# Optimization experiments

Measured on AMD Instinct MI355X. Metric: run time of the kernel, lower is better.

## Reference

```python
import jax, jax.numpy as jnp
import numpy as np
import math

B, L, D = 2, 2048, 2048
H = 16
HD = D // H  # 128
EPS = 1e-8
ROPE_BASE = 10000.0


def _rms(x, g):
    return x * jax.lax.rsqrt(jnp.mean(x * x, axis=-1, keepdims=True) + EPS) * g


def _rope_tables(seq_len, head_dim, dtype):
    inv_freq = 1.0 / (ROPE_BASE ** (jnp.arange(0, head_dim, 2, dtype=jnp.float32) / head_dim))
    t = jnp.arange(seq_len, dtype=jnp.float32)
    freqs = jnp.outer(t, inv_freq)                 # [L, HD/2]
    emb = jnp.concatenate([freqs, freqs], axis=-1)  # [L, HD]
    return jnp.cos(emb).astype(dtype), jnp.sin(emb).astype(dtype)


def _rotate_half(x):
    x1, x2 = jnp.split(x, 2, axis=-1)
    return jnp.concatenate([-x2, x1], axis=-1)


def setup_inputs() -> dict:
    key = jax.random.key(0)
    ks = jax.random.split(key, 4)
    s = 0.02
    return {
        'x': jax.random.normal(ks[0], (B, L, D), jnp.float32),
        'Wqkv': jax.random.normal(ks[1], (D, 3 * D), jnp.float32) * s,
        'bqkv': jnp.zeros((3 * D,), jnp.float32),
        'Wo': jax.random.normal(ks[2], (D, D), jnp.float32) * s,
        'bo': jnp.zeros((D,), jnp.float32),
        'g1': jnp.ones((D,), jnp.float32),
        'g2': jnp.ones((D,), jnp.float32),
        'Wp': jax.random.normal(ks[3], (D, 8 * D), jnp.float32) * s,
        'bp': jnp.zeros((8 * D,), jnp.float32),
        'Wff_out': jax.random.normal(jax.random.fold_in(key, 7), (4 * D, D), jnp.float32) * s,
        'bff_out': jnp.zeros((D,), jnp.float32),
    }


def reference(x, Wqkv, bqkv, Wo, bo, g1, g2, Wp, bp, Wff_out, bff_out):
    b, l, d = x.shape
    # pre-norm + fused QKV projection
    h = _rms(x, g1)
    qkv = h @ Wqkv + bqkv                                  # [B, L, 3D]
    q, k, v = jnp.split(qkv, 3, axis=-1)
    def heads(t):
        return t.reshape(b, l, H, HD).transpose(0, 2, 1, 3)  # [B, H, L, HD]
    q, k, v = heads(q), heads(k), heads(v)
    # RoPE
    cos, sin = _rope_tables(l, HD, x.dtype)                 # [L, HD]
    cos = cos[None, None]
    sin = sin[None, None]
    q = q * cos + _rotate_half(q) * sin
    k = k * cos + _rotate_half(k) * sin
    # causal SDPA
    scale = 1.0 / math.sqrt(HD)
    scores = jnp.einsum('bhqd,bhkd->bhqk', q, k) * scale
    causal = jnp.tril(jnp.ones((l, l), dtype=bool))
    scores = jnp.where(causal[None, None], scores, jnp.finfo(scores.dtype).min)
    attn = jax.nn.softmax(scores, axis=-1)
    o = jnp.einsum('bhqk,bhkd->bhqd', attn, v)              # [B, H, L, HD]
    o = o.transpose(0, 2, 1, 3).reshape(b, l, d)
    attn_out = o @ Wo + bo
    x = x + attn_out                                        # residual (dropout=0, eval)
    # SwiGLU FFN, pre-norm
    h2 = _rms(x, g2)
    p = h2 @ Wp + bp                                        # [B, L, 8D]
    gate, value = jnp.split(p, 2, axis=-1)
    ff = (jax.nn.silu(gate) * value) @ Wff_out + bff_out
    return x + ff
```

## Files before the change

### kernel.cpp

```cpp
#include <hip/hip_runtime.h>
#include <stdint.h>

typedef unsigned short u16;
typedef float floatx4 __attribute__((ext_vector_type(4)));
typedef short bf16x8 __attribute__((ext_vector_type(8)));

#define DEVI __device__ __forceinline__

#define B_ 2
#define L_ 2048
#define D_ 2048
#define H_ 16
#define HD_ 128
#define M_ 4096

DEVI u16 f2bf(float f) {
  union { float f; uint32_t u; } v; v.f = f;
  uint32_t r = v.u + 0x7fffu + ((v.u >> 16) & 1u);
  return (u16)(r >> 16);
}
DEVI float bf2f(u16 h) {
  union { uint32_t u; float f; } v; v.u = ((uint32_t)h) << 16;
  return v.f;
}

DEVI floatx4 mfma16(bf16x8 a, bf16x8 b, floatx4 c) {
  return __builtin_amdgcn_mfma_f32_16x16x32_bf16(a, b, c, 0, 0, 0);
}

DEVI void gl2lds16(const u16* g, u16* l) {
  __builtin_amdgcn_global_load_lds((const __attribute__((address_space(1))) void*)g,
                                   (__attribute__((address_space(3))) void*)l, 16, 0, 0);
}

__global__ void rmsnorm_kernel(const float* __restrict__ x, const float* __restrict__ g,
                               u16* __restrict__ out) {
  int row = blockIdx.x;
  int tid = threadIdx.x;
  const float* xr = x + (size_t)row * D_;
  float4 v0 = ((const float4*)xr)[tid];
  float4 v1 = ((const float4*)xr)[256 + tid];
  float ss = v0.x*v0.x + v0.y*v0.y + v0.z*v0.z + v0.w*v0.w
           + v1.x*v1.x + v1.y*v1.y + v1.z*v1.z + v1.w*v1.w;
  #pragma unroll
  for (int off = 32; off > 0; off >>= 1) ss += __shfl_xor(ss, off, 64);
  __shared__ float red[4];
  int wv = tid >> 6, ln = tid & 63;
  if (ln == 0) red[wv] = ss;
  __syncthreads();
  float tot = red[0] + red[1] + red[2] + red[3];
  float scale = rsqrtf(tot * (1.0f / (float)D_) + 1e-8f);
  float4 g0 = ((const float4*)g)[tid];
  float4 g1v = ((const float4*)g)[256 + tid];
  u16* orow = out + (size_t)row * D_;
  ushort4 o0, o1;
  o0.x = f2bf(v0.x * scale * g0.x);  o0.y = f2bf(v0.y * scale * g0.y);
  o0.z = f2bf(v0.z * scale * g0.z);  o0.w = f2bf(v0.w * scale * g0.w);
  o1.x = f2bf(v1.x * scale * g1v.x); o1.y = f2bf(v1.y * scale * g1v.y);
  o1.z = f2bf(v1.z * scale * g1v.z); o1.w = f2bf(v1.w * scale * g1v.w);
  ((ushort4*)orow)[tid] = o0;
  ((ushort4*)orow)[256 + tid] = o1;
}

__global__ void transpose_w_kernel(const float* __restrict__ W, u16* __restrict__ Wt,
                                   int Kd, int Nd) {
  __shared__ float tile[32][33];
  int n0 = blockIdx.x * 32, k0 = blockIdx.y * 32;
  int tid = threadIdx.x;
  int r = tid >> 3, c4 = (tid & 7) * 4;
  float4 v = *(const float4*)(W + (size_t)(k0 + r) * Nd + n0 + c4);
  tile[r][c4 + 0] = v.x; tile[r][c4 + 1] = v.y; tile[r][c4 + 2] = v.z; tile[r][c4 + 3] = v.w;
  __syncthreads();
  ushort4 o;
  o.x = f2bf(tile[c4 + 0][r]); o.y = f2bf(tile[c4 + 1][r]);
  o.z = f2bf(tile[c4 + 2][r]); o.w = f2bf(tile[c4 + 3][r]);
  *(ushort4*)(Wt + (size_t)(n0 + r) * Kd + k0 + c4) = o;
}

__global__ void rope_qk_kernel(const u16* __restrict__ qkv, u16* __restrict__ q_r,
                               u16* __restrict__ k_r) {
  int idx = blockIdx.x * 256 + threadIdx.x;
  int i = idx & 63;
  int h = (idx >> 6) & (H_ - 1);
  int l = (idx >> 10) & (L_ - 1);
  int b = idx >> 21;
  float freq = expf(-(float)i * 0.14391156831212787f);
  float ang = (float)l * freq;
  float s, c;
  sincosf(ang, &s, &c);
  size_t base_in = (size_t)(b * L_ + l) * (3 * D_);
  size_t qi = base_in + h * HD_ + i;
  size_t ki = base_in + D_ + h * HD_ + i;
  float q1 = bf2f(qkv[qi]), q2 = bf2f(qkv[qi + 64]);
  float k1 = bf2f(qkv[ki]), k2 = bf2f(qkv[ki + 64]);
  size_t base_out = ((size_t)(b * H_ + h) * L_ + l) * HD_ + i;
  q_r[base_out]      = f2bf(q1 * c - q2 * s);
  q_r[base_out + 64] = f2bf(q2 * c + q1 * s);
  k_r[base_out]      = f2bf(k1 * c - k2 * s);
  k_r[base_out + 64] = f2bf(k2 * c + k1 * s);
}

__global__ void v_transpose_kernel(const u16* __restrict__ qkv, u16* __restrict__ vt) {
  __shared__ u16 tile[32][36];
  int bh = blockIdx.z;
  int d0 = blockIdx.y * 32;
  int l0 = blockIdx.x * 32;
  int b = bh >> 4, h = bh & 15;
  int tid = threadIdx.x;
  int r = tid >> 3, c4 = (tid & 7) * 4;
  const u16* src = qkv + (size_t)(b * L_ + l0 + r) * (3 * D_) + 2 * D_ + h * HD_ + d0 + c4;
  ushort4 v = *(const ushort4*)src;
  tile[r][c4 + 0] = v.x; tile[r][c4 + 1] = v.y; tile[r][c4 + 2] = v.z; tile[r][c4 + 3] = v.w;
  __syncthreads();
  ushort4 o;
  o.x = tile[c4 + 0][r]; o.y = tile[c4 + 1][r]; o.z = tile[c4 + 2][r]; o.w = tile[c4 + 3][r];
  *(ushort4*)(vt + ((size_t)bh * HD_ + d0 + r) * L_ + l0 + c4) = o;
}


template <int MODE>
__launch_bounds__(256, 3)
__global__ void gemm_bt_kernel(const u16* __restrict__ A, const u16* __restrict__ Bt,
                               const float* __restrict__ bias,
                               const float* __restrict__ resid,
                               void* __restrict__ out, int Nn, int Kk) {
  __shared__ __attribute__((aligned(16))) u16 As[128 * 64];
  __shared__ __attribute__((aligned(16))) u16 Bs[128 * 64];
  int tid = threadIdx.x;
  int wave = tid >> 6, lane = tid & 63, quad = lane >> 4, lr = lane & 15;
  int m0 = blockIdx.y * 128, n0 = blockIdx.x * 128;
  int wm = (wave >> 1) * 64, wn = (wave & 1) * 64;
  floatx4 acc[4][4];
  floatx4 z4 = {0.f, 0.f, 0.f, 0.f};
  #pragma unroll
  for (int i = 0; i < 4; i++)
    #pragma unroll
    for (int j = 0; j < 4; j++) acc[i][j] = z4;
  int dr8 = tid >> 3;
  int dg = ((tid & 7) ^ (dr8 & 7)) * 8;
  const u16* Ap = A + (size_t)m0 * Kk;
  const u16* Bp = Bt + (size_t)n0 * Kk;
  for (int kt = 0; kt < Kk; kt += 64) {
    __syncthreads();
    #pragma unroll
    for (int p = 0; p < 4; p++)
      gl2lds16(Ap + (size_t)(p * 32 + dr8) * Kk + kt + dg, As + p * 2048 + tid * 8);
    #pragma unroll
    for (int p = 0; p < 4; p++)
      gl2lds16(Bp + (size_t)(p * 32 + dr8) * Kk + kt + dg, Bs + p * 2048 + tid * 8);
    __syncthreads();
    #pragma unroll
    for (int kk = 0; kk < 2; ++kk) {
      int swz = ((kk * 4 + quad) ^ (lr & 7)) * 8;
      bf16x8 af[4], bfr[4];
      #pragma unroll
      for (int i = 0; i < 4; i++)
        af[i] = *(const bf16x8*)&As[(wm + i * 16 + lr) * 64 + swz];
      #pragma unroll
      for (int i = 0; i < 4; i++)
        bfr[i] = *(const bf16x8*)&Bs[(wn + i * 16 + lr) * 64 + swz];
      #pragma unroll
      for (int mi = 0; mi < 4; mi++)
        #pragma unroll
        for (int ni = 0; ni < 4; ni++)
          acc[mi][ni] = mfma16(af[mi], bfr[ni], acc[mi][ni]);
    }
  }
  #pragma unroll
  for (int mi = 0; mi < 4; mi++) {
    #pragma unroll
    for (int ni = 0; ni < 4; ni++) {
      int col = n0 + wn + ni * 16 + lr;
      float bcol = bias[col];
      #pragma unroll
      for (int r2 = 0; r2 < 4; r2++) {
        int row = m0 + wm + mi * 16 + quad * 4 + r2;
        float v = acc[mi][ni][r2] + bcol;
        size_t off = (size_t)row * Nn + col;
        if (MODE == 0) {
          ((u16*)out)[off] = f2bf(v);
        } else {
          ((float*)out)[off] = v + resid[off];
        }
      }
    }
  }
}

__launch_bounds__(256, 2)
__global__ void ffn_gemm_kernel(const u16* __restrict__ A, const u16* __restrict__ Wt,
                                const float* __restrict__ bp,
                                u16* __restrict__ out, int Kk) {
  __shared__ __attribute__((aligned(16))) u16 As[128 * 64];
  __shared__ __attribute__((aligned(16))) u16 Bg[128 * 64];
  __shared__ __attribute__((aligned(16))) u16 Bv[128 * 64];
  int tid = threadIdx.x;
  int wave = tid >> 6, lane = tid & 63, quad = lane >> 4, lr = lane & 15;
  int m0 = blockIdx.y * 128, n0 = blockIdx.x * 128;
  int wm = (wave >> 1) * 64, wn = (wave & 1) * 64;
  floatx4 accg[4][4], accv[4][4];
  floatx4 z4 = {0.f, 0.f, 0.f, 0.f};
  #pragma unroll
  for (int i = 0; i < 4; i++)
    #pragma unroll
    for (int j = 0; j < 4; j++) { accg[i][j] = z4; accv[i][j] = z4; }
  int dr8 = tid >> 3;
  int dg = ((tid & 7) ^ (dr8 & 7)) * 8;
  const u16* Ap = A + (size_t)m0 * Kk;
  const u16* Bgp = Wt + (size_t)n0 * Kk;
  const u16* Bvp = Wt + (size_t)(8192 + n0) * Kk;
  for (int kt = 0; kt < Kk; kt += 64) {
    __syncthreads();
    #pragma unroll
    for (int p = 0; p < 4; p++)
      gl2lds16(Ap + (size_t)(p * 32 + dr8) * Kk + kt + dg, As + p * 2048 + tid * 8);
    #pragma unroll
    for (int p = 0; p < 4; p++)
      gl2lds16(Bgp + (size_t)(p * 32 + dr8) * Kk + kt + dg, Bg + p * 2048 + tid * 8);
    #pragma unroll
    for (int p = 0; p < 4; p++)
      gl2lds16(Bvp + (size_t)(p * 32 + dr8) * Kk + kt + dg, Bv + p * 2048 + tid * 8);
    __syncthreads();
    #pragma unroll
    for (int kk = 0; kk < 2; ++kk) {
      int swz = ((kk * 4 + quad) ^ (lr & 7)) * 8;
      bf16x8 af[4], bgf[4], bvf[4];
      #pragma unroll
      for (int i = 0; i < 4; i++) {
        af[i]  = *(const bf16x8*)&As[(wm + i * 16 + lr) * 64 + swz];
        bgf[i] = *(const bf16x8*)&Bg[(wn + i * 16 + lr) * 64 + swz];
        bvf[i] = *(const bf16x8*)&Bv[(wn + i * 16 + lr) * 64 + swz];
      }
      #pragma unroll
      for (int mi = 0; mi < 4; mi++)
        #pragma unroll
        for (int ni = 0; ni < 4; ni++) {
          accg[mi][ni] = mfma16(af[mi], bgf[ni], accg[mi][ni]);
          accv[mi][ni] = mfma16(af[mi], bvf[ni], accv[mi][ni]);
        }
    }
  }
  #pragma unroll
  for (int mi = 0; mi < 4; mi++) {
    #pragma unroll
    for (int ni = 0; ni < 4; ni++) {
      int col = n0 + wn + ni * 16 + lr;
      float bg = bp[col], bv = bp[col + 8192];
      #pragma unroll
      for (int r2 = 0; r2 < 4; r2++) {
        int row = m0 + wm + mi * 16 + quad * 4 + r2;
        float gv = accg[mi][ni][r2] + bg;
        float vv = accv[mi][ni][r2] + bv;
        float sg = gv / (1.f + __expf(-gv));
        out[(size_t)row * 8192 + col] = f2bf(sg * vv);
      }
    }
  }
}

__launch_bounds__(256, 2)
__global__ void attn_kernel(const u16* __restrict__ q_r, const u16* __restrict__ k_r,
                            const u16* __restrict__ vt, u16* __restrict__ o) {
  __shared__ __attribute__((aligned(16))) u16 KPs[128 * 128];
  __shared__ __attribute__((aligned(16))) u16 Vs[128 * 128];
  int bh = blockIdx.y, b = bh >> 4, h = bh & 15;
  int qt = (blockIdx.y < 16) ? blockIdx.x : (15 - blockIdx.x);
  int q0 = qt * 128;
  int tid = threadIdx.x, wave = tid >> 6, lane = tid & 63, quad = lane >> 4, lr = lane & 15;
  int wq0 = wave * 32;
  const u16* Qp = q_r + (size_t)bh * L_ * HD_;
  const u16* Kp = k_r + (size_t)bh * L_ * HD_;
  const u16* Vtp = vt + (size_t)bh * HD_ * L_;
  const float scale = 0.08838834764831845f;
  bf16x8 qf[2][4];
  #pragma unroll
  for (int mi = 0; mi < 2; mi++)
    #pragma unroll
    for (int kk = 0; kk < 4; kk++)
      qf[mi][kk] = *(const bf16x8*)(Qp + (size_t)(q0 + wq0 + mi * 16 + lr) * HD_ + kk * 32 + quad * 8);
  float mrun[2][4], lrun[2][4];
  floatx4 z4 = {0.f, 0.f, 0.f, 0.f};
  floatx4 oacc[2][8];
  #pragma unroll
  for (int mi = 0; mi < 2; mi++) {
    #pragma unroll
    for (int r2 = 0; r2 < 4; r2++) { mrun[mi][r2] = -__builtin_inff(); lrun[mi][r2] = 0.f; }
    #pragma unroll
    for (int di = 0; di < 8; di++) oacc[mi][di] = z4;
  }
  int dr = tid >> 4;
  int dgo = ((tid & 15) ^ dr) * 8;
  for (int jt = 0; jt <= qt; ++jt) {
    __syncthreads();
    #pragma unroll
    for (int p = 0; p < 8; ++p) {
      int r = p * 16 + dr;
      gl2lds16(Kp + (size_t)(jt * 128 + r) * HD_ + dgo, KPs + p * 2048 + tid * 8);
      gl2lds16(Vtp + (size_t)r * L_ + jt * 128 + dgo,   Vs + p * 2048 + tid * 8);
    }
    __syncthreads();
    floatx4 sacc[2][8];
    #pragma unroll
    for (int mi = 0; mi < 2; mi++)
      #pragma unroll
      for (int ni = 0; ni < 8; ni++) sacc[mi][ni] = z4;
    #pragma unroll
    for (int kk = 0; kk < 4; ++kk) {
      bf16x8 kf[8];
      #pragma unroll
      for (int ni = 0; ni < 8; ++ni)
        kf[ni] = *(const bf16x8*)&KPs[(ni * 16 + lr) * 128 + ((kk * 4 + quad) ^ lr) * 8];
      #pragma unroll
      for (int mi = 0; mi < 2; mi++)
        #pragma unroll
        for (int ni = 0; ni < 8; ni++)
          sacc[mi][ni] = mfma16(qf[mi][kk], kf[ni], sacc[mi][ni]);
    }
    __syncthreads();
    bool diag = (jt == qt);
    #pragma unroll
    for (int mi = 0; mi < 2; mi++) {
      #pragma unroll
      for (int r2 = 0; r2 < 4; r2++) {
        int row_abs = q0 + wq0 + mi * 16 + quad * 4 + r2;
        int prow = wq0 + mi * 16 + quad * 4 + r2;
        float sv[8];
        float mloc = -__builtin_inff();
        #pragma unroll
        for (int ni = 0; ni < 8; ni++) {
          float v = sacc[mi][ni][r2] * scale;
          if (diag && (jt * 128 + ni * 16 + lr) > row_abs) v = -__builtin_inff();
          sv[ni] = v;
          mloc = fmaxf(mloc, v);
        }
        #pragma unroll
        for (int off = 1; off < 16; off <<= 1) mloc = fmaxf(mloc, __shfl_xor(mloc, off, 16));
        float mold = mrun[mi][r2];
        float mnew = fmaxf(mold, mloc);
        float alpha = __expf(mold - mnew);
        float ls = 0.f;
        #pragma unroll
        for (int ni = 0; ni < 8; ni++) {
          float p = __expf(sv[ni] - mnew);
          ls += p;
          int slot = (ni * 2 + (lr >> 3)) ^ (prow & 15);
          KPs[prow * 128 + slot * 8 + (lr & 7)] = f2bf(p);
        }
        #pragma unroll
        for (int off = 1; off < 16; off <<= 1) ls += __shfl_xor(ls, off, 16);
        lrun[mi][r2] = lrun[mi][r2] * alpha + ls;
        mrun[mi][r2] = mnew;
        #pragma unroll
        for (int di = 0; di < 8; di++) oacc[mi][di][r2] *= alpha;
      }
    }
    #pragma unroll
    for (int kk = 0; kk < 4; ++kk) {
      bf16x8 pf[2], vf[8];
      #pragma unroll
      for (int mi = 0; mi < 2; mi++)
        pf[mi] = *(const bf16x8*)&KPs[(wq0 + mi * 16 + lr) * 128 + ((kk * 4 + quad) ^ lr) * 8];
      #pragma unroll
      for (int di = 0; di < 8; di++)
        vf[di] = *(const bf16x8*)&Vs[(di * 16 + lr) * 128 + ((kk * 4 + quad) ^ lr) * 8];
      #pragma unroll
      for (int mi = 0; mi < 2; mi++)
        #pragma unroll
        for (int di = 0; di < 8; di++)
          oacc[mi][di] = mfma16(pf[mi], vf[di], oacc[mi][di]);
    }
  }
  #pragma unroll
  for (int mi = 0; mi < 2; mi++) {
    #pragma unroll
    for (int r2 = 0; r2 < 4; r2++) {
      float inv = 1.f / lrun[mi][r2];
      int l_abs = q0 + wq0 + mi * 16 + quad * 4 + r2;
      size_t base = (size_t)(b * L_ + l_abs) * D_ + h * HD_;
      #pragma unroll
      for (int di = 0; di < 8; di++)
        o[base + di * 16 + lr] = f2bf(oacc[mi][di][r2] * inv);
    }
  }
}

extern "C" void kernel_launch(void* const* d_in, const int* in_sizes, int n_in,
                              void* d_out, int out_size, void* d_ws, size_t ws_size,
                              hipStream_t stream) {
  const float* x    = (const float*)d_in[0];
  const float* Wqkv = (const float*)d_in[1];
  const float* bqkv = (const float*)d_in[2];
  const float* Wo   = (const float*)d_in[3];
  const float* bo   = (const float*)d_in[4];
  const float* g1   = (const float*)d_in[5];
  const float* g2   = (const float*)d_in[6];
  const float* Wp   = (const float*)d_in[7];
  const float* bp   = (const float*)d_in[8];
  const float* Wff  = (const float*)d_in[9];
  const float* bff  = (const float*)d_in[10];
  char* ws = (char*)d_ws;
  u16*  wbuf = (u16*)(ws);
  u16*  hbuf = (u16*)(ws + 67108864);
  float* x1  = (float*)(ws + 83886080);
  char* rA = ws + 117440512;
  u16* qkv  = (u16*)(rA);
  u16* q_r  = (u16*)(rA + 50331648);
  u16* k_r  = (u16*)(rA + 67108864);
  u16* vtb  = (u16*)(rA + 83886080);
  u16* ob   = (u16*)(rA + 100663296);
  u16* ffin = (u16*)(rA);
  float* outp = (float*)d_out;
  dim3 blk(256);

  rmsnorm_kernel<<<M_, blk, 0, stream>>>(x, g1, hbuf);
  transpose_w_kernel<<<dim3(6144 / 32, 2048 / 32), blk, 0, stream>>>(Wqkv, wbuf, 2048, 6144);
  gemm_bt_kernel<0><<<dim3(48, 32), blk, 0, stream>>>(hbuf, wbuf, bqkv, nullptr, qkv, 6144, 2048);
  rope_qk_kernel<<<(B_ * L_ * H_ * 64) / 256, blk, 0, stream>>>(qkv, q_r, k_r);
  v_transpose_kernel<<<dim3(L_ / 32, HD_ / 32, B_ * H_), blk, 0, stream>>>(qkv, vtb);
  attn_kernel<<<dim3(L_ / 128, B_ * H_), blk, 0, stream>>>(q_r, k_r, vtb, ob);
  transpose_w_kernel<<<dim3(2048 / 32, 2048 / 32), blk, 0, stream>>>(Wo, wbuf, 2048, 2048);
  gemm_bt_kernel<1><<<dim3(16, 32), blk, 0, stream>>>(ob, wbuf, bo, x, x1, 2048, 2048);
  rmsnorm_kernel<<<M_, blk, 0, stream>>>(x1, g2, hbuf);
  transpose_w_kernel<<<dim3(16384 / 32, 2048 / 32), blk, 0, stream>>>(Wp, wbuf, 2048, 16384);
  ffn_gemm_kernel<<<dim3(64, 32), blk, 0, stream>>>(hbuf, wbuf, bp, ffin, 2048);
  transpose_w_kernel<<<dim3(2048 / 32, 8192 / 32), blk, 0, stream>>>(Wff, wbuf, 8192, 2048);
  gemm_bt_kernel<1><<<dim3(16, 32), blk, 0, stream>>>(ffin, wbuf, bff, x1, outp, 2048, 8192);
}
```

Before: 1.068 ms.

## Double-buffer LDS tiles in GEMM, FFN and attention kernels with prefetch

Splits LDS into two buffers in the generic GEMM, the SwiGLU FFN GEMM and the attention kernel. The next K (or key) tile is prefetched into the spare buffer while the current one is consumed, leaving one barrier per iteration instead of two. The FFN GEMM narrows its N tile to 64 and doubles the grid, and attention moves from 128-key to 64-key tiles with a separate P buffer, masking every tile. The larger LDS footprint cuts the generic GEMM's launch-bounds occupancy from 3 to 2 blocks, and the smaller tiles mean more loop iterations and reloads.

Measured after the change: 1.079 ms. Within noise of the previous version (+1.0%).

```diff
diff --git a/kernel.cpp b/kernel.cpp
--- a/kernel.cpp
+++ b/kernel.cpp
@@ -119,13 +119,13 @@
 
 
 template <int MODE>
-__launch_bounds__(256, 3)
+__launch_bounds__(256, 2)
 __global__ void gemm_bt_kernel(const u16* __restrict__ A, const u16* __restrict__ Bt,
                                const float* __restrict__ bias,
                                const float* __restrict__ resid,
                                void* __restrict__ out, int Nn, int Kk) {
-  __shared__ __attribute__((aligned(16))) u16 As[128 * 64];
-  __shared__ __attribute__((aligned(16))) u16 Bs[128 * 64];
+  __shared__ __attribute__((aligned(16))) u16 As[2][128 * 64];
+  __shared__ __attribute__((aligned(16))) u16 Bs[2][128 * 64];
   int tid = threadIdx.x;
   int wave = tid >> 6, lane = tid & 63, quad = lane >> 4, lr = lane & 15;
   int m0 = blockIdx.y * 128, n0 = blockIdx.x * 128;
@@ -140,31 +140,41 @@
   int dg = ((tid & 7) ^ (dr8 & 7)) * 8;
   const u16* Ap = A + (size_t)m0 * Kk;
   const u16* Bp = Bt + (size_t)n0 * Kk;
+  #pragma unroll
+  for (int p = 0; p < 4; p++) {
+    gl2lds16(Ap + (size_t)(p * 32 + dr8) * Kk + dg, As[0] + p * 2048 + tid * 8);
+    gl2lds16(Bp + (size_t)(p * 32 + dr8) * Kk + dg, Bs[0] + p * 2048 + tid * 8);
+  }
+  int cur = 0;
   for (int kt = 0; kt < Kk; kt += 64) {
     __syncthreads();
-    #pragma unroll
-    for (int p = 0; p < 4; p++)
-      gl2lds16(Ap + (size_t)(p * 32 + dr8) * Kk + kt + dg, As + p * 2048 + tid * 8);
-    #pragma unroll
-    for (int p = 0; p < 4; p++)
-      gl2lds16(Bp + (size_t)(p * 32 + dr8) * Kk + kt + dg, Bs + p * 2048 + tid * 8);
-    __syncthreads();
+    if (kt + 64 < Kk) {
+      int nx = cur ^ 1;
+      #pragma unroll
+      for (int p = 0; p < 4; p++) {
+        gl2lds16(Ap + (size_t)(p * 32 + dr8) * Kk + (kt + 64) + dg, As[nx] + p * 2048 + tid * 8);
+        gl2lds16(Bp + (size_t)(p * 32 + dr8) * Kk + (kt + 64) + dg, Bs[nx] + p * 2048 + tid * 8);
+      }
+    }
+    const u16* Asc = As[cur];
+    const u16* Bsc = Bs[cur];
     #pragma unroll
     for (int kk = 0; kk < 2; ++kk) {
       int swz = ((kk * 4 + quad) ^ (lr & 7)) * 8;
       bf16x8 af[4], bfr[4];
       #pragma unroll
       for (int i = 0; i < 4; i++)
-        af[i] = *(const bf16x8*)&As[(wm + i * 16 + lr) * 64 + swz];
+        af[i] = *(const bf16x8*)&Asc[(wm + i * 16 + lr) * 64 + swz];
       #pragma unroll
       for (int i = 0; i < 4; i++)
-        bfr[i] = *(const bf16x8*)&Bs[(wn + i * 16 + lr) * 64 + swz];
+        bfr[i] = *(const bf16x8*)&Bsc[(wn + i * 16 + lr) * 64 + swz];
       #pragma unroll
       for (int mi = 0; mi < 4; mi++)
         #pragma unroll
         for (int ni = 0; ni < 4; ni++)
           acc[mi][ni] = mfma16(af[mi], bfr[ni], acc[mi][ni]);
     }
+    cur ^= 1;
   }
   #pragma unroll
   for (int mi = 0; mi < 4; mi++) {
@@ -191,66 +201,82 @@
 __global__ void ffn_gemm_kernel(const u16* __restrict__ A, const u16* __restrict__ Wt,
                                 const float* __restrict__ bp,
                                 u16* __restrict__ out, int Kk) {
-  __shared__ __attribute__((aligned(16))) u16 As[128 * 64];
-  __shared__ __attribute__((aligned(16))) u16 Bg[128 * 64];
-  __shared__ __attribute__((aligned(16))) u16 Bv[128 * 64];
+  __shared__ __attribute__((aligned(16))) u16 As[2][128 * 64];
+  __shared__ __attribute__((aligned(16))) u16 Bg[2][64 * 64];
+  __shared__ __attribute__((aligned(16))) u16 Bv[2][64 * 64];
   int tid = threadIdx.x;
   int wave = tid >> 6, lane = tid & 63, quad = lane >> 4, lr = lane & 15;
-  int m0 = blockIdx.y * 128, n0 = blockIdx.x * 128;
-  int wm = (wave >> 1) * 64, wn = (wave & 1) * 64;
-  floatx4 accg[4][4], accv[4][4];
+  int m0 = blockIdx.y * 128, n0 = blockIdx.x * 64;
+  int wm = (wave >> 1) * 64, wn = (wave & 1) * 32;
+  floatx4 accg[4][2], accv[4][2];
   floatx4 z4 = {0.f, 0.f, 0.f, 0.f};
   #pragma unroll
   for (int i = 0; i < 4; i++)
     #pragma unroll
-    for (int j = 0; j < 4; j++) { accg[i][j] = z4; accv[i][j] = z4; }
+    for (int j = 0; j < 2; j++) { accg[i][j] = z4; accv[i][j] = z4; }
   int dr8 = tid >> 3;
   int dg = ((tid & 7) ^ (dr8 & 7)) * 8;
   const u16* Ap = A + (size_t)m0 * Kk;
   const u16* Bgp = Wt + (size_t)n0 * Kk;
   const u16* Bvp = Wt + (size_t)(8192 + n0) * Kk;
+  #pragma unroll
+  for (int p = 0; p < 4; p++)
+    gl2lds16(Ap + (size_t)(p * 32 + dr8) * Kk + dg, As[0] + p * 2048 + tid * 8);
+  #pragma unroll
+  for (int p = 0; p < 2; p++) {
+    gl2lds16(Bgp + (size_t)(p * 32 + dr8) * Kk + dg, Bg[0] + p * 2048 + tid * 8);
+    gl2lds16(Bvp + (size_t)(p * 32 + dr8) * Kk + dg, Bv[0] + p * 2048 + tid * 8);
+  }
+  int cur = 0;
   for (int kt = 0; kt < Kk; kt += 64) {
     __syncthreads();
-    #pragma unroll
-    for (int p = 0; p < 4; p++)
-      gl2lds16(Ap + (size_t)(p * 32 + dr8) * Kk + kt + dg, As + p * 2048 + tid * 8);
-    #pragma unroll
-    for (int p = 0; p < 4; p++)
-      gl2lds16(Bgp + (size_t)(p * 32 + dr8) * Kk + kt + dg, Bg + p * 2048 + tid * 8);
-    #pragma unroll
-    for (int p = 0; p < 4; p++)
-      gl2lds16(Bvp + (size_t)(p * 32 + dr8) * Kk + kt + dg, Bv + p * 2048 + tid * 8);
-    __syncthreads();
+    if (kt + 64 < Kk) {
+      int nx = cur ^ 1;
+      #pragma unroll
+      for (int p = 0; p < 4; p++)
+        gl2lds16(Ap + (size_t)(p * 32 + dr8) * Kk + (kt + 64) + dg, As[nx] + p * 2048 + tid * 8);
+      #pragma unroll
+      for (int p = 0; p < 2; p++) {
+        gl2lds16(Bgp + (size_t)(p * 32 + dr8) * Kk + (kt + 64) + dg, Bg[nx] + p * 2048 + tid * 8);
+        gl2lds16(Bvp + (size_t)(p * 32 + dr8) * Kk + (kt + 64) + dg, Bv[nx] + p * 2048 + tid * 8);
+      }
+    }
+    const u16* Asc = As[cur];
+    const u16* Bgc = Bg[cur];
+    const u16* Bvc = Bv[cur];
     #pragma unroll
     for (int kk = 0; kk < 2; ++kk) {
       int swz = ((kk * 4 + quad) ^ (lr & 7)) * 8;
-      bf16x8 af[4], bgf[4], bvf[4];
-      #pragma unroll
-      for (int i = 0; i < 4; i++) {
-        af[i]  = *(const bf16x8*)&As[(wm + i * 16 + lr) * 64 + swz];
-        bgf[i] = *(const bf16x8*)&Bg[(wn + i * 16 + lr) * 64 + swz];
-        bvf[i] = *(const bf16x8*)&Bv[(wn + i * 16 + lr) * 64 + swz];
+      bf16x8 af[4], bgf[2], bvf[2];
+      #pragma unroll
+      for (int i = 0; i < 4; i++)
+        af[i]  = *(const bf16x8*)&Asc[(wm + i * 16 + lr) * 64 + swz];
+      #pragma unroll
+      for (int i = 0; i < 2; i++) {
+        bgf[i] = *(const bf16x8*)&Bgc[(wn + i * 16 + lr) * 64 + swz];
+        bvf[i] = *(const bf16x8*)&Bvc[(wn + i * 16 + lr) * 64 + swz];
       }
       #pragma unroll
       for (int mi = 0; mi < 4; mi++)
         #pragma unroll
-        for (int ni = 0; ni < 4; ni++) {
+        for (int ni = 0; ni < 2; ni++) {
           accg[mi][ni] = mfma16(af[mi], bgf[ni], accg[mi][ni]);
           accv[mi][ni] = mfma16(af[mi], bvf[ni], accv[mi][ni]);
         }
     }
+    cur ^= 1;
   }
   #pragma unroll
   for (int mi = 0; mi < 4; mi++) {
     #pragma unroll
-    for (int ni = 0; ni < 4; ni++) {
+    for (int ni = 0; ni < 2; ni++) {
       int col = n0 + wn + ni * 16 + lr;
-      float bg = bp[col], bv = bp[col + 8192];
+      float bgc = bp[col], bvc = bp[col + 8192];
       #pragma unroll
       for (int r2 = 0; r2 < 4; r2++) {
         int row = m0 + wm + mi * 16 + quad * 4 + r2;
-        float gv = accg[mi][ni][r2] + bg;
-        float vv = accv[mi][ni][r2] + bv;
+        float gv = accg[mi][ni][r2] + bgc;
+        float vv = accv[mi][ni][r2] + bvc;
         float sg = gv / (1.f + __expf(-gv));
         out[(size_t)row * 8192 + col] = f2bf(sg * vv);
       }
@@ -261,8 +287,9 @@
 __launch_bounds__(256, 2)
 __global__ void attn_kernel(const u16* __restrict__ q_r, const u16* __restrict__ k_r,
                             const u16* __restrict__ vt, u16* __restrict__ o) {
-  __shared__ __attribute__((aligned(16))) u16 KPs[128 * 128];
-  __shared__ __attribute__((aligned(16))) u16 Vs[128 * 128];
+  __shared__ __attribute__((aligned(16))) u16 Ks[2][64 * 128];
+  __shared__ __attribute__((aligned(16))) u16 Vs[2][128 * 64];
+  __shared__ __attribute__((aligned(16))) u16 Ps[128 * 64];
   int bh = blockIdx.y, b = bh >> 4, h = bh & 15;
   int qt = (blockIdx.y < 16) ? blockIdx.x : (15 - blockIdx.x);
   int q0 = qt * 128;
@@ -288,48 +315,60 @@
     #pragma unroll
     for (int di = 0; di < 8; di++) oacc[mi][di] = z4;
   }
-  int dr = tid >> 4;
-  int dgo = ((tid & 15) ^ dr) * 8;
-  for (int jt = 0; jt <= qt; ++jt) {
+  int dr16 = tid >> 4;
+  int dg16 = ((tid & 15) ^ dr16) * 8;
+  int dr8 = tid >> 3;
+  int dg8 = ((tid & 7) ^ (dr8 & 7)) * 8;
+  int J = 2 * (qt + 1);
+  #pragma unroll
+  for (int p = 0; p < 4; ++p) {
+    gl2lds16(Kp + (size_t)(p * 16 + dr16) * HD_ + dg16, Ks[0] + p * 2048 + tid * 8);
+    gl2lds16(Vtp + (size_t)(p * 32 + dr8) * L_ + dg8,   Vs[0] + p * 2048 + tid * 8);
+  }
+  int cur = 0;
+  for (int j = 0; j < J; ++j) {
+    int k0a = j * 64;
     __syncthreads();
-    #pragma unroll
-    for (int p = 0; p < 8; ++p) {
-      int r = p * 16 + dr;
-      gl2lds16(Kp + (size_t)(jt * 128 + r) * HD_ + dgo, KPs + p * 2048 + tid * 8);
-      gl2lds16(Vtp + (size_t)r * L_ + jt * 128 + dgo,   Vs + p * 2048 + tid * 8);
-    }
-    __syncthreads();
-    floatx4 sacc[2][8];
+    if (j + 1 < J) {
+      int nx = cur ^ 1;
+      int k1 = k0a + 64;
+      #pragma unroll
+      for (int p = 0; p < 4; ++p) {
+        gl2lds16(Kp + (size_t)(k1 + p * 16 + dr16) * HD_ + dg16, Ks[nx] + p * 2048 + tid * 8);
+        gl2lds16(Vtp + (size_t)(p * 32 + dr8) * L_ + k1 + dg8,   Vs[nx] + p * 2048 + tid * 8);
+      }
+    }
+    const u16* Kc = Ks[cur];
+    const u16* Vc = Vs[cur];
+    floatx4 sacc[2][4];
     #pragma unroll
     for (int mi = 0; mi < 2; mi++)
       #pragma unroll
-      for (int ni = 0; ni < 8; ni++) sacc[mi][ni] = z4;
+      for (int ni = 0; ni < 4; ni++) sacc[mi][ni] = z4;
     #pragma unroll
     for (int kk = 0; kk < 4; ++kk) {
-      bf16x8 kf[8];
-      #pragma unroll
-      for (int ni = 0; ni < 8; ++ni)
-        kf[ni] = *(const bf16x8*)&KPs[(ni * 16 + lr) * 128 + ((kk * 4 + quad) ^ lr) * 8];
+      bf16x8 kf[4];
+      #pragma unroll
+      for (int ni = 0; ni < 4; ++ni)
+        kf[ni] = *(const bf16x8*)&Kc[(ni * 16 + lr) * 128 + ((kk * 4 + quad) ^ lr) * 8];
       #pragma unroll
       for (int mi = 0; mi < 2; mi++)
         #pragma unroll
-        for (int ni = 0; ni < 8; ni++)
+        for (int ni = 0; ni < 4; ni++)
           sacc[mi][ni] = mfma16(qf[mi][kk], kf[ni], sacc[mi][ni]);
     }
-    __syncthreads();
-    bool diag = (jt == qt);
     #pragma unroll
     for (int mi = 0; mi < 2; mi++) {
       #pragma unroll
       for (int r2 = 0; r2 < 4; r2++) {
         int row_abs = q0 + wq0 + mi * 16 + quad * 4 + r2;
         int prow = wq0 + mi * 16 + quad * 4 + r2;
-        float sv[8];
+        float sv[4];
         float mloc = -__builtin_inff();
         #pragma unroll
-        for (int ni = 0; ni < 8; ni++) {
+        for (int ni = 0; ni < 4; ni++) {
           float v = sacc[mi][ni][r2] * scale;
-          if (diag && (jt * 128 + ni * 16 + lr) > row_abs) v = -__builtin_inff();
+          if ((k0a + ni * 16 + lr) > row_abs) v = -__builtin_inff();
           sv[ni] = v;
           mloc = fmaxf(mloc, v);
         }
@@ -340,11 +379,11 @@
         float alpha = __expf(mold - mnew);
         float ls = 0.f;
         #pragma unroll
-        for (int ni = 0; ni < 8; ni++) {
+        for (int ni = 0; ni < 4; ni++) {
           float p = __expf(sv[ni] - mnew);
           ls += p;
-          int slot = (ni * 2 + (lr >> 3)) ^ (prow & 15);
-          KPs[prow * 128 + slot * 8 + (lr & 7)] = f2bf(p);
+          int slot = (ni * 2 + (lr >> 3)) ^ (prow & 7);
+          Ps[prow * 64 + slot * 8 + (lr & 7)] = f2bf(p);
         }
         #pragma unroll
         for (int off = 1; off < 16; off <<= 1) ls += __shfl_xor(ls, off, 16);
@@ -355,20 +394,22 @@
       }
     }
     #pragma unroll
-    for (int kk = 0; kk < 4; ++kk) {
+    for (int kk = 0; kk < 2; ++kk) {
+      int swz = ((kk * 4 + quad) ^ (lr & 7)) * 8;
       bf16x8 pf[2], vf[8];
       #pragma unroll
       for (int mi = 0; mi < 2; mi++)
-        pf[mi] = *(const bf16x8*)&KPs[(wq0 + mi * 16 + lr) * 128 + ((kk * 4 + quad) ^ lr) * 8];
+        pf[mi] = *(const bf16x8*)&Ps[(wq0 + mi * 16 + lr) * 64 + swz];
       #pragma unroll
       for (int di = 0; di < 8; di++)
-        vf[di] = *(const bf16x8*)&Vs[(di * 16 + lr) * 128 + ((kk * 4 + quad) ^ lr) * 8];
+        vf[di] = *(const bf16x8*)&Vc[(di * 16 + lr) * 64 + swz];
       #pragma unroll
       for (int mi = 0; mi < 2; mi++)
         #pragma unroll
         for (int di = 0; di < 8; di++)
           oacc[mi][di] = mfma16(pf[mi], vf[di], oacc[mi][di]);
     }
+    cur ^= 1;
   }
   #pragma unroll
   for (int mi = 0; mi < 2; mi++) {
@@ -422,7 +463,7 @@
   gemm_bt_kernel<1><<<dim3(16, 32), blk, 0, stream>>>(ob, wbuf, bo, x, x1, 2048, 2048);
   rmsnorm_kernel<<<M_, blk, 0, stream>>>(x1, g2, hbuf);
   transpose_w_kernel<<<dim3(16384 / 32, 2048 / 32), blk, 0, stream>>>(Wp, wbuf, 2048, 16384);
-  ffn_gemm_kernel<<<dim3(64, 32), blk, 0, stream>>>(hbuf, wbuf, bp, ffin, 2048);
+  ffn_gemm_kernel<<<dim3(128, 32), blk, 0, stream>>>(hbuf, wbuf, bp, ffin, 2048);
   transpose_w_kernel<<<dim3(2048 / 32, 8192 / 32), blk, 0, stream>>>(Wff, wbuf, 8192, 2048);
   gemm_bt_kernel<1><<<dim3(16, 32), blk, 0, stream>>>(ffin, wbuf, bff, x1, outp, 2048, 8192);
 }
```
